# Kernel optimization log

Measured on AMD Instinct MI355X. Metric: run time of the kernel, lower is better.

## Reference

```python
import jax, jax.numpy as jnp
import numpy as np
from jax.ops import segment_sum, segment_max

N_M = 100000   # muon nodes
N_J = 100000   # jet nodes
E   = 1600000  # edges per relation (~avg degree 16)
D   = 64       # input feature dim
H   = 64       # hidden_channels
C   = 2        # num_classes

def setup_inputs():
    key = jax.random.key(0)
    ks = jax.random.split(key, 16)
    g = lambda k, shape, fan: jax.random.normal(k, shape, jnp.float32) / np.sqrt(fan).astype(np.float32)
    return {
        "x_muons": jax.random.normal(ks[0], (N_M, D), jnp.float32),
        "x_jets":  jax.random.normal(ks[1], (N_J, D), jnp.float32),
        "ei_mm": jax.random.randint(ks[2], (2, E), 0, N_M, jnp.int32),
        "ei_mj": jnp.stack([jax.random.randint(ks[3], (E,), 0, N_M, jnp.int32),
                            jax.random.randint(ks[4], (E,), 0, N_J, jnp.int32)]),
        "ei_jj": jax.random.randint(ks[5], (2, E), 0, N_J, jnp.int32),
        "gat_w_src": g(ks[6], (D, H), D),
        "gat_w_dst": g(ks[7], (D, H), D),
        "gat_att_src": g(ks[8], (H,), H),
        "gat_att_dst": g(ks[9], (H,), H),
        "gat_bias": jnp.zeros((H,), jnp.float32),
        "sage_w_l": g(ks[10], (D, H), D),
        "sage_w_r": g(ks[11], (D, H), D),
        "sage_bias": jnp.zeros((H,), jnp.float32),
        "gcn_w": g(ks[12], (D, H), D),
        "gcn_bias": jnp.zeros((H,), jnp.float32),
        "lin_w": g(ks[13], (H, C), H),
        "lin_b": jnp.zeros((C,), jnp.float32),
    }

def _add_self_loops(ei, n):
    loop = jnp.arange(n, dtype=ei.dtype)
    return jnp.concatenate([ei[0], loop]), jnp.concatenate([ei[1], loop])

def _gat(x, ei, w_src, w_dst, att_src, att_dst, bias):
    # PyG GATConv, heads=1, add_self_loops=True, negative_slope=0.2
    n = x.shape[0]
    src, dst = _add_self_loops(ei, n)
    hs = x @ w_src                      # [n, H] source-side messages
    hd = x @ w_dst                      # dst-side (attention only)
    a = jax.nn.leaky_relu((hs @ att_src)[src] + (hd @ att_dst)[dst], 0.2)
    m = segment_max(a, dst, num_segments=n)      # per-dst softmax (stable)
    ea = jnp.exp(a - m[dst])
    z = segment_sum(ea, dst, num_segments=n)
    alpha = ea / z[dst]                 # self loop guarantees z > 0
    return segment_sum(alpha[:, None] * hs[src], dst, num_segments=n) + bias

def _sage(x_src, x_dst, ei, w_l, w_r, bias):
    # PyG SAGEConv: mean aggregation, root weight, no self loops
    n = x_dst.shape[0]
    src, dst = ei[0], ei[1]
    agg = segment_sum(x_src[src], dst, num_segments=n)
    cnt = segment_sum(jnp.ones_like(dst, jnp.float32), dst, num_segments=n)
    mean = agg / jnp.maximum(cnt, 1.0)[:, None]
    return mean @ w_l + x_dst @ w_r + bias

def _gcn(x, ei, w, bias):
    # PyG GCNConv: symmetric gcn_norm on A + I
    n = x.shape[0]
    src, dst = _add_self_loops(ei, n)
    xw = x @ w
    deg = segment_sum(jnp.ones_like(dst, jnp.float32), dst, num_segments=n)
    dis = deg ** -0.5                   # deg >= 1 due to self loops
    norm = dis[src] * dis[dst]
    return segment_sum(norm[:, None] * xw[src], dst, num_segments=n) + bias

def reference(x_muons, x_jets, ei_mm, ei_mj, ei_jj,
              gat_w_src, gat_w_dst, gat_att_src, gat_att_dst, gat_bias,
              sage_w_l, sage_w_r, sage_bias, gcn_w, gcn_bias, lin_w, lin_b):
    # Original forward returns inside the layer loop -> exactly one HeteroConv layer runs.
    muons = _gat(x_muons, ei_mm, gat_w_src, gat_w_dst, gat_att_src, gat_att_dst, gat_bias)
    jets = (_sage(x_muons, x_jets, ei_mj, sage_w_l, sage_w_r, sage_bias)
            + _gcn(x_jets, ei_jj, gcn_w, gcn_bias))   # HeteroConv aggr='sum' on dst type 'jets'
    muons = jax.nn.relu(muons)
    jets = jax.nn.relu(jets)
    out = jnp.concatenate([muons, jets], axis=0)       # [N_M + N_J, H]
    return jax.nn.sigmoid(out @ lin_w + lin_b)
```

## Files before the change

### kernel.cpp

```cpp
#include <hip/hip_runtime.h>
#include <math.h>

#define N_M 100000
#define N_J 100000
#define NE  1600000
#define NTOT (3*N_M)
#define ETOT (3*NE)
#define NB_SCAN 293
#define DD  64
#define HH  64

#define NBIN 586
#define BIN_SHIFT 9
#define G1 640
#define EPB ((ETOT + G1 - 1) / G1)

__device__ __forceinline__ float lrelu(float a){ return fmaxf(a, 0.2f*a); }
__device__ __forceinline__ float wmax(float v){
    #pragma unroll
    for (int o = 32; o; o >>= 1) v = fmaxf(v, __shfl_xor(v, o));
    return v;
}
__device__ __forceinline__ float wsum(float v){
    #pragma unroll
    for (int o = 32; o; o >>= 1) v += __shfl_xor(v, o);
    return v;
}
__device__ __forceinline__ float sigm(float x){ return 1.f/(1.f + expf(-x)); }

__device__ __forceinline__ unsigned short f2bf(float f){
    unsigned u = __float_as_uint(f);
    u += 0x7FFFu + ((u >> 16) & 1u);
    return (unsigned short)(u >> 16);
}
__device__ __forceinline__ float bf2f(unsigned short h){
    return __uint_as_float((unsigned)h << 16);
}


__global__ __launch_bounds__(256) void k_muon_prep(
    const float* __restrict__ x, const float* __restrict__ w_src,
    const float* __restrict__ w_dst, const float* __restrict__ att_src,
    const float* __restrict__ att_dst,
    unsigned short* __restrict__ hs_b, float* __restrict__ as_, float* __restrict__ ad_,
    unsigned short* __restrict__ xm_b)
{
    __shared__ float lw[DD*HH];
    __shared__ float latt[HH];
    __shared__ float lvd[DD];
    int tid = threadIdx.x;
    for (int i = tid; i < DD*HH; i += 256) lw[i] = w_src[i];
    if (tid < HH) latt[tid] = att_src[tid];
    if (tid < DD){
        float s = 0.f;
        #pragma unroll 8
        for (int h = 0; h < HH; ++h) s += w_dst[tid*HH + h] * att_dst[h];
        lvd[tid] = s;
    }
    __syncthreads();
    int row = blockIdx.x*64 + (tid >> 2);
    int q = tid & 3;
    if (row >= N_M) return;
    const float4* x4 = (const float4*)(x + (size_t)row*DD);
    float acc[16];
    #pragma unroll
    for (int f = 0; f < 16; ++f) acc[f] = 0.f;
    float adp = 0.f;
    for (int kk = 0; kk < 16; ++kk){
        float4 xv = x4[kk];
        adp += xv.x*lvd[4*kk] + xv.y*lvd[4*kk+1] + xv.z*lvd[4*kk+2] + xv.w*lvd[4*kk+3];
        if ((kk >> 2) == q)
            *(ushort4*)(xm_b + (size_t)row*DD + 4*kk) =
                make_ushort4(f2bf(xv.x), f2bf(xv.y), f2bf(xv.z), f2bf(xv.w));
        float xs[4] = {xv.x, xv.y, xv.z, xv.w};
        #pragma unroll
        for (int j = 0; j < 4; ++j){
            const float* wp = lw + (4*kk + j)*HH + (q << 4);
            float xk = xs[j];
            #pragma unroll
            for (int f = 0; f < 16; ++f) acc[f] = fmaf(xk, wp[f], acc[f]);
        }
    }
    float asp = 0.f;
    #pragma unroll
    for (int f = 0; f < 16; ++f) asp += acc[f] * latt[(q<<4) + f];
    asp += __shfl_xor(asp, 1);
    asp += __shfl_xor(asp, 2);
    unsigned short* hp = hs_b + (size_t)row*HH + (q << 4);
    #pragma unroll
    for (int j = 0; j < 4; ++j)
        ((ushort4*)hp)[j] = make_ushort4(f2bf(acc[4*j]), f2bf(acc[4*j+1]),
                                         f2bf(acc[4*j+2]), f2bf(acc[4*j+3]));
    if (q == 0){ as_[row] = asp; ad_[row] = adp; }
}

__global__ __launch_bounds__(256) void k_jet_prep(
    const float* __restrict__ x, const float* __restrict__ gcn_w,
    const float* __restrict__ w_r, const float* __restrict__ sb,
    const float* __restrict__ gb,
    unsigned short* __restrict__ xw_b, float* __restrict__ xr)
{
    __shared__ float lwg[DD*HH];
    __shared__ float lwr[DD*HH];
    __shared__ float lb[HH];
    int tid = threadIdx.x;
    for (int i = tid; i < DD*HH; i += 256){ lwg[i] = gcn_w[i]; lwr[i] = w_r[i]; }
    if (tid < HH) lb[tid] = sb[tid] + gb[tid];
    __syncthreads();
    int row = blockIdx.x*64 + (tid >> 2);
    int q = tid & 3;
    if (row >= N_J) return;
    const float4* x4 = (const float4*)(x + (size_t)row*DD);
    float accg[16], accr[16];
    #pragma unroll
    for (int f = 0; f < 16; ++f){ accg[f] = 0.f; accr[f] = 0.f; }
    for (int kk = 0; kk < 16; ++kk){
        float4 xv = x4[kk];
        float xs[4] = {xv.x, xv.y, xv.z, xv.w};
        #pragma unroll
        for (int j = 0; j < 4; ++j){
            const float* wg = lwg + (4*kk + j)*HH + (q << 4);
            const float* wr = lwr + (4*kk + j)*HH + (q << 4);
            float xk = xs[j];
            #pragma unroll
            for (int f = 0; f < 16; ++f){
                accg[f] = fmaf(xk, wg[f], accg[f]);
                accr[f] = fmaf(xk, wr[f], accr[f]);
            }
        }
    }
    unsigned short* hp = xw_b + (size_t)row*HH + (q << 4);
    float* rp = xr + (size_t)row*HH + (q << 4);
    #pragma unroll
    for (int j = 0; j < 4; ++j){
        ((ushort4*)hp)[j] = make_ushort4(f2bf(accg[4*j]), f2bf(accg[4*j+1]),
                                         f2bf(accg[4*j+2]), f2bf(accg[4*j+3]));
        int f0 = (q << 4) + 4*j;
        ((float4*)rp)[j] = make_float4(accr[4*j]   + lb[f0],
                                       accr[4*j+1] + lb[f0+1],
                                       accr[4*j+2] + lb[f0+2],
                                       accr[4*j+3] + lb[f0+3]);
    }
}


__device__ __forceinline__ void edge_rd(int t, const int* ei_mm, const int* ei_mj,
                                        const int* ei_jj, const int** ei, int* r, int* e){
    if (t < NE){ *r = 0; *e = t; *ei = ei_mm; }
    else if (t < 2*NE){ *r = 1; *e = t - NE; *ei = ei_mj; }
    else { *r = 2; *e = t - 2*NE; *ei = ei_jj; }
}

__global__ __launch_bounds__(256) void k_bin0(
    const int* __restrict__ ei_mm, const int* __restrict__ ei_mj,
    const int* __restrict__ ei_jj, int* __restrict__ g_bincnt)
{
    __shared__ int bh[NBIN];
    int tid = threadIdx.x;
    for (int i = tid; i < NBIN; i += 256) bh[i] = 0;
    __syncthreads();
    int t0 = blockIdx.x * EPB;
    int t1 = min(t0 + EPB, ETOT);
    for (int t = t0 + tid; t < t1; t += 256){
        const int* ei; int r, e;
        edge_rd(t, ei_mm, ei_mj, ei_jj, &ei, &r, &e);
        int bucket = r*N_M + ei[NE + e];
        atomicAdd(&bh[bucket >> BIN_SHIFT], 1);
    }
    __syncthreads();
    for (int i = tid; i < NBIN; i += 256)
        if (bh[i]) atomicAdd(&g_bincnt[i], bh[i]);
}

__global__ void k_binscan(const int* __restrict__ g_bincnt, int* __restrict__ g_binoff,
                          int* __restrict__ g_bincur, int* __restrict__ offs)
{
    int l = threadIdx.x;
    int base = l * 10;
    int v[10]; int s = 0;
    #pragma unroll
    for (int k = 0; k < 10; ++k){
        int idx = base + k;
        v[k] = (idx < NBIN) ? g_bincnt[idx] : 0;
        s += v[k];
    }
    int inc = s;
    #pragma unroll
    for (int o = 1; o < 64; o <<= 1){
        int u = __shfl_up(inc, o);
        if (l >= o) inc += u;
    }
    int ex = inc - s;
    #pragma unroll
    for (int k = 0; k < 10; ++k){
        int idx = base + k;
        if (idx < NBIN){ g_binoff[idx] = ex; g_bincur[idx] = ex; ex += v[k]; }
    }
    if (l == 63) g_binoff[NBIN] = ex;
    if (l == 0)  offs[NTOT] = ETOT;
}

__global__ __launch_bounds__(256) void k_bin1(
    const int* __restrict__ ei_mm, const int* __restrict__ ei_mj,
    const int* __restrict__ ei_jj, int* __restrict__ g_bincur,
    unsigned* __restrict__ binned)
{
    __shared__ int bh[NBIN];
    __shared__ int cb[NBIN];
    int tid = threadIdx.x;
    for (int i = tid; i < NBIN; i += 256) bh[i] = 0;
    __syncthreads();
    int t0 = blockIdx.x * EPB;
    int t1 = min(t0 + EPB, ETOT);
    for (int t = t0 + tid; t < t1; t += 256){
        const int* ei; int r, e;
        edge_rd(t, ei_mm, ei_mj, ei_jj, &ei, &r, &e);
        int bucket = r*N_M + ei[NE + e];
        atomicAdd(&bh[bucket >> BIN_SHIFT], 1);
    }
    __syncthreads();
    for (int i = tid; i < NBIN; i += 256){
        int c = bh[i];
        cb[i] = c ? atomicAdd(&g_bincur[i], c) : 0;
        bh[i] = 0;
    }
    __syncthreads();
    for (int t = t0 + tid; t < t1; t += 256){
        const int* ei; int r, e;
        edge_rd(t, ei_mm, ei_mj, ei_jj, &ei, &r, &e);
        int s = ei[e];
        int bucket = r*N_M + ei[NE + e];
        int bin = bucket >> BIN_SHIFT;
        int lb  = bucket & 511;
        int pos = cb[bin] + atomicAdd(&bh[bin], 1);
        binned[pos] = ((unsigned)lb << 17) | (unsigned)s;
    }
}

__global__ __launch_bounds__(256) void k_build(
    const unsigned* __restrict__ binned, const int* __restrict__ g_binoff,
    int* __restrict__ offs, int* __restrict__ perm, float* __restrict__ dis)
{
    __shared__ int lh[512];
    __shared__ int lcur[512];
    __shared__ int ls[256];
    int b = blockIdx.x, tid = threadIdx.x;
    int e0 = g_binoff[b], e1 = g_binoff[b+1];
    lh[tid] = 0; lh[tid + 256] = 0;
    __syncthreads();
    for (int e = e0 + tid; e < e1; e += 256)
        atomicAdd(&lh[binned[e] >> 17], 1);
    __syncthreads();
    int a0 = lh[2*tid], a1 = lh[2*tid + 1];
    int s = a0 + a1;
    ls[tid] = s; __syncthreads();
    for (int o = 1; o < 256; o <<= 1){
        int u = (tid >= o) ? ls[tid - o] : 0;
        __syncthreads();
        ls[tid] += u;
        __syncthreads();
    }
    int ex = ls[tid] - s;
    lcur[2*tid]     = ex;
    lcur[2*tid + 1] = ex + a0;
    int gb = b*512 + 2*tid;
    if (gb     < NTOT) offs[gb]     = e0 + ex;
    if (gb + 1 < NTOT) offs[gb + 1] = e0 + ex + a0;
    if (gb     >= 2*N_M && gb     < NTOT) dis[gb     - 2*N_M] = rsqrtf((float)a0 + 1.f);
    if (gb + 1 >= 2*N_M && gb + 1 < NTOT) dis[gb + 1 - 2*N_M] = rsqrtf((float)a1 + 1.f);
    __syncthreads();
    for (int e = e0 + tid; e < e1; e += 256){
        unsigned p = binned[e];
        int pos = atomicAdd(&lcur[p >> 17], 1);
        perm[e0 + pos] = (int)(p & 0x1FFFFu);
    }
}


__global__ void k_hist(const int* __restrict__ ei_mm, const int* __restrict__ ei_mj,
                       const int* __restrict__ ei_jj, int* __restrict__ cnt){
    int t = blockIdx.x*256 + threadIdx.x;
    if (t >= ETOT) return;
    const int* ei; int r, e;
    edge_rd(t, ei_mm, ei_mj, ei_jj, &ei, &r, &e);
    atomicAdd(&cnt[r*N_M + ei[NE + e]], 1);
}

__global__ __launch_bounds__(256) void k_scan1(const int* __restrict__ cnt,
                                               int* __restrict__ offs, int* __restrict__ bsum){
    __shared__ int ls[256];
    int b = blockIdx.x, t = threadIdx.x;
    int base = b*1024 + t*4;
    int4 c = make_int4(0,0,0,0);
    if (base < NTOT) c = *(const int4*)(cnt + base);
    int s = c.x + c.y + c.z + c.w;
    ls[t] = s; __syncthreads();
    for (int o = 1; o < 256; o <<= 1){
        int a = (t >= o) ? ls[t - o] : 0;
        __syncthreads();
        ls[t] += a;
        __syncthreads();
    }
    int excl = ls[t] - s;
    if (t == 255) bsum[b] = ls[255];
    if (base < NTOT){
        offs[base]   = excl;
        offs[base+1] = excl + c.x;
        offs[base+2] = excl + c.x + c.y;
        offs[base+3] = excl + c.x + c.y + c.z;
    }
}

__global__ __launch_bounds__(512) void k_scan2(int* __restrict__ bsum){
    __shared__ int ls[512];
    int t = threadIdx.x;
    int v = (t < NB_SCAN) ? bsum[t] : 0;
    ls[t] = v; __syncthreads();
    for (int o = 1; o < 512; o <<= 1){
        int a = (t >= o) ? ls[t - o] : 0;
        __syncthreads();
        ls[t] += a;
        __syncthreads();
    }
    if (t < NB_SCAN) bsum[t] = ls[t] - v;
}

__global__ void k_scan3(int* __restrict__ offs, const int* __restrict__ bsum){
    int b = blockIdx.x, t = threadIdx.x;
    int base = b*1024 + t*4;
    if (base >= NTOT) return;
    int add = bsum[b];
    int4* p = (int4*)(offs + base);
    int4 v = *p;
    v.x += add; v.y += add; v.z += add; v.w += add;
    *p = v;
}

__global__ void k_fill(const int* __restrict__ ei_mm, const int* __restrict__ ei_mj,
                       const int* __restrict__ ei_jj, const int* __restrict__ offs,
                       int* __restrict__ cursor, int* __restrict__ perm){
    int t = blockIdx.x*256 + threadIdx.x;
    if (t >= ETOT) return;
    const int* ei; int r, e;
    edge_rd(t, ei_mm, ei_mj, ei_jj, &ei, &r, &e);
    int s = ei[e];
    int bkt = r*N_M + ei[NE + e];
    int pos = atomicAdd(&cursor[bkt], 1);
    perm[offs[bkt] + pos] = s;
}

__global__ void k_set_offs_top(int* __restrict__ offs){ offs[NTOT] = ETOT; }

__global__ void k_dis(const int* __restrict__ offs, float* __restrict__ dis){
    int j = blockIdx.x*256 + threadIdx.x;
    if (j >= N_J) return;
    int beg = offs[2*N_M + j];
    int end = (j == N_J-1) ? ETOT : offs[2*N_M + j + 1];
    dis[j] = rsqrtf((float)(end - beg + 1));
}


__global__ __launch_bounds__(512) void k_muon_gat_out(
    const int* __restrict__ offs, const int* __restrict__ perm,
    const float* __restrict__ as_, const float* __restrict__ ad_,
    const unsigned short* __restrict__ hs_b, const float* __restrict__ gat_bias,
    const float* __restrict__ lin_w, const float* __restrict__ lin_b,
    float* __restrict__ out)
{
    int wid = threadIdx.x >> 6;
    int l = threadIdx.x & 63;
    int d = blockIdx.x*8 + wid;
    if (d >= N_M) return;
    int p = l & 15, g = l >> 4;
    int beg = offs[d], end = offs[d+1];
    float ad_d = ad_[d];
    float a_self = lrelu(as_[d] + ad_d);
    float m = a_self, z = 0.f;
    float acc0 = 0.f, acc1 = 0.f, acc2 = 0.f, acc3 = 0.f;
    for (int base = beg; base < end; base += 64){
        int e = base + l;
        int sB = 0; float aB = -1e30f;
        if (e < end){ sB = perm[e]; aB = lrelu(as_[sB] + ad_d); }
        float bm = wmax(aB);
        if (bm > m){
            float sc = expf(m - bm);
            acc0 *= sc; acc1 *= sc; acc2 *= sc; acc3 *= sc; z *= sc;
            m = bm;
        }
        float eaB = expf(aB - m);
        z += wsum(eaB);
        int cc = min(64, end - base);
        int k = 0;
        for (; k + 32 <= cc; k += 32){
            #pragma unroll
            for (int qq = 0; qq < 8; ++qq){
                int idx = k + qq*4 + g;
                int s = __shfl(sB, idx);
                float w = __shfl(eaB, idx);
                ushort4 v = *(const ushort4*)(hs_b + (size_t)s*HH + 4*p);
                acc0 = fmaf(w, bf2f(v.x), acc0);
                acc1 = fmaf(w, bf2f(v.y), acc1);
                acc2 = fmaf(w, bf2f(v.z), acc2);
                acc3 = fmaf(w, bf2f(v.w), acc3);
            }
        }
        for (; k < cc; k += 4){
            int idx = k + g;
            int cl = min(idx, cc - 1);
            int s = __shfl(sB, cl);
            float w = __shfl(eaB, cl);
            if (idx >= cc) w = 0.f;
            ushort4 v = *(const ushort4*)(hs_b + (size_t)s*HH + 4*p);
            acc0 = fmaf(w, bf2f(v.x), acc0);
            acc1 = fmaf(w, bf2f(v.y), acc1);
            acc2 = fmaf(w, bf2f(v.z), acc2);
            acc3 = fmaf(w, bf2f(v.w), acc3);
        }
    }
    acc0 += __shfl_xor(acc0, 16); acc0 += __shfl_xor(acc0, 32);
    acc1 += __shfl_xor(acc1, 16); acc1 += __shfl_xor(acc1, 32);
    acc2 += __shfl_xor(acc2, 16); acc2 += __shfl_xor(acc2, 32);
    acc3 += __shfl_xor(acc3, 16); acc3 += __shfl_xor(acc3, 32);
    float eself = expf(a_self - m);
    z += eself;
    ushort4 hv = *(const ushort4*)(hs_b + (size_t)d*HH + 4*p);
    acc0 = fmaf(eself, bf2f(hv.x), acc0);
    acc1 = fmaf(eself, bf2f(hv.y), acc1);
    acc2 = fmaf(eself, bf2f(hv.z), acc2);
    acc3 = fmaf(eself, bf2f(hv.w), acc3);
    float rz = 1.f / z;
    float q0 = 0.f, q1 = 0.f;
    {
        float a[4] = {acc0, acc1, acc2, acc3};
        #pragma unroll
        for (int c = 0; c < 4; ++c){
            int f = 4*p + c;
            float v2 = fmaxf(a[c]*rz + gat_bias[f], 0.f);
            q0 = fmaf(v2, lin_w[f*2 + 0], q0);
            q1 = fmaf(v2, lin_w[f*2 + 1], q1);
        }
    }
    #pragma unroll
    for (int o = 1; o <= 8; o <<= 1){ q0 += __shfl_xor(q0, o); q1 += __shfl_xor(q1, o); }
    if (l == 0){
        size_t oo = (size_t)d*2;
        out[oo]   = sigm(q0 + lin_b[0]);
        out[oo+1] = sigm(q1 + lin_b[1]);
    }
}

__global__ __launch_bounds__(512) void k_jet_out(
    const unsigned short* __restrict__ xm_b, const unsigned short* __restrict__ xw_b,
    const float* __restrict__ xr, const float* __restrict__ dis,
    const int* __restrict__ offs, const int* __restrict__ perm,
    const float* __restrict__ w_l,
    const float* __restrict__ lin_w, const float* __restrict__ lin_b,
    float* __restrict__ out)
{
    __shared__ float lwl[DD*HH];
    int tid = threadIdx.x;
    for (int i = tid; i < DD*HH; i += 512) lwl[i] = w_l[i];
    __syncthreads();
    int wid = tid >> 6;
    int l = tid & 63;
    int j = blockIdx.x*8 + wid;
    if (j >= N_J) return;
    int p = l & 15, g = l >> 4;
    int beg1 = offs[N_M + j],  end1 = offs[N_M + j + 1];
    int beg2 = offs[2*N_M + j];
    int end2 = (j == N_J-1) ? ETOT : offs[2*N_M + j + 1];
    float dj = dis[j];
    float sa0 = 0.f, sa1 = 0.f, sa2 = 0.f, sa3 = 0.f;
    float gc0 = 0.f, gc1 = 0.f, gc2 = 0.f, gc3 = 0.f;
    for (int b1 = beg1, b2 = beg2; b1 < end1 || b2 < end2; b1 += 64, b2 += 64){
        int e1 = b1 + l, e2 = b2 + l;
        bool h1 = (b1 < end1), h2 = (b2 < end2);
        int sB1 = 0, sB2 = 0; float nB2 = 0.f;
        if (h1 && e1 < end1) sB1 = perm[e1];
        if (h2 && e2 < end2){ sB2 = perm[e2]; nB2 = dis[sB2]*dj; }
        if (h1){
            int cc = min(64, end1 - b1);
            int k = 0;
            for (; k + 16 <= cc; k += 16){
                #pragma unroll
                for (int qq = 0; qq < 4; ++qq){
                    int idx = k + qq*4 + g;
                    int s = __shfl(sB1, idx);
                    ushort4 v = *(const ushort4*)(xm_b + (size_t)s*DD + 4*p);
                    sa0 += bf2f(v.x); sa1 += bf2f(v.y); sa2 += bf2f(v.z); sa3 += bf2f(v.w);
                }
            }
            for (; k < cc; k += 4){
                int idx = k + g;
                int cl = min(idx, cc - 1);
                int s = __shfl(sB1, cl);
                float w = (idx < cc) ? 1.f : 0.f;
                ushort4 v = *(const ushort4*)(xm_b + (size_t)s*DD + 4*p);
                sa0 = fmaf(w, bf2f(v.x), sa0);
                sa1 = fmaf(w, bf2f(v.y), sa1);
                sa2 = fmaf(w, bf2f(v.z), sa2);
                sa3 = fmaf(w, bf2f(v.w), sa3);
            }
        }
        if (h2){
            int cc = min(64, end2 - b2);
            int k = 0;
            for (; k + 16 <= cc; k += 16){
                #pragma unroll
                for (int qq = 0; qq < 4; ++qq){
                    int idx = k + qq*4 + g;
                    int s = __shfl(sB2, idx);
                    float w = __shfl(nB2, idx);
                    ushort4 v = *(const ushort4*)(xw_b + (size_t)s*HH + 4*p);
                    gc0 = fmaf(w, bf2f(v.x), gc0);
                    gc1 = fmaf(w, bf2f(v.y), gc1);
                    gc2 = fmaf(w, bf2f(v.z), gc2);
                    gc3 = fmaf(w, bf2f(v.w), gc3);
                }
            }
            for (; k < cc; k += 4){
                int idx = k + g;
                int cl = min(idx, cc - 1);
                int s = __shfl(sB2, cl);
                float w = __shfl(nB2, cl);
                if (idx >= cc) w = 0.f;
                ushort4 v = *(const ushort4*)(xw_b + (size_t)s*HH + 4*p);
                gc0 = fmaf(w, bf2f(v.x), gc0);
                gc1 = fmaf(w, bf2f(v.y), gc1);
                gc2 = fmaf(w, bf2f(v.z), gc2);
                gc3 = fmaf(w, bf2f(v.w), gc3);
            }
        }
    }
    sa0 += __shfl_xor(sa0, 16); sa0 += __shfl_xor(sa0, 32);
    sa1 += __shfl_xor(sa1, 16); sa1 += __shfl_xor(sa1, 32);
    sa2 += __shfl_xor(sa2, 16); sa2 += __shfl_xor(sa2, 32);
    sa3 += __shfl_xor(sa3, 16); sa3 += __shfl_xor(sa3, 32);
    gc0 += __shfl_xor(gc0, 16); gc0 += __shfl_xor(gc0, 32);
    gc1 += __shfl_xor(gc1, 16); gc1 += __shfl_xor(gc1, 32);
    gc2 += __shfl_xor(gc2, 16); gc2 += __shfl_xor(gc2, 32);
    gc3 += __shfl_xor(gc3, 16); gc3 += __shfl_xor(gc3, 32);
    float inv = (end1 > beg1) ? 1.f/(float)(end1 - beg1) : 1.f;
    float mean_a[4] = {sa0*inv, sa1*inv, sa2*inv, sa3*inv};
    {
        ushort4 sv = *(const ushort4*)(xw_b + (size_t)j*HH + 4*p);
        float djj = dj*dj;
        gc0 = fmaf(djj, bf2f(sv.x), gc0);
        gc1 = fmaf(djj, bf2f(sv.y), gc1);
        gc2 = fmaf(djj, bf2f(sv.z), gc2);
        gc3 = fmaf(djj, bf2f(sv.w), gc3);
    }
    float b0 = __shfl(gc0, l >> 2), b1 = __shfl(gc1, l >> 2);
    float b2 = __shfl(gc2, l >> 2), b3 = __shfl(gc3, l >> 2);
    int c2 = l & 3;
    float accg_lin = (c2 == 0) ? b0 : ((c2 == 1) ? b1 : ((c2 == 2) ? b2 : b3));
    float xacc = 0.f;
    #pragma unroll
    for (int k = 0; k < 64; ++k){
        float mk = __shfl(mean_a[k & 3], k >> 2);
        xacc = fmaf(mk, lwl[k*64 + l], xacc);
    }
    float v2 = fmaxf(xacc + accg_lin + xr[(size_t)j*HH + l], 0.f);
    float q0 = wsum(v2 * lin_w[l*2 + 0]);
    float q1 = wsum(v2 * lin_w[l*2 + 1]);
    if (l == 0){
        size_t oo = (size_t)(N_M + j)*2;
        out[oo]   = sigm(q0 + lin_b[0]);
        out[oo+1] = sigm(q1 + lin_b[1]);
    }
}

extern "C" void kernel_launch(void* const* d_in, const int* in_sizes, int n_in,
                              void* d_out, int out_size, void* d_ws, size_t ws_size,
                              hipStream_t stream) {
    const float* x_muons   = (const float*)d_in[0];
    const float* x_jets    = (const float*)d_in[1];
    const int*   ei_mm     = (const int*)d_in[2];
    const int*   ei_mj     = (const int*)d_in[3];
    const int*   ei_jj     = (const int*)d_in[4];
    const float* gat_w_src = (const float*)d_in[5];
    const float* gat_w_dst = (const float*)d_in[6];
    const float* gat_att_s = (const float*)d_in[7];
    const float* gat_att_d = (const float*)d_in[8];
    const float* gat_bias  = (const float*)d_in[9];
    const float* sage_w_l  = (const float*)d_in[10];
    const float* sage_w_r  = (const float*)d_in[11];
    const float* sage_bias = (const float*)d_in[12];
    const float* gcn_w     = (const float*)d_in[13];
    const float* gcn_bias  = (const float*)d_in[14];
    const float* lin_w     = (const float*)d_in[15];
    const float* lin_b     = (const float*)d_in[16];
    float* out = (float*)d_out;

    float* ws = (float*)d_ws;
    size_t o = 0;
    unsigned short* hs_b = (unsigned short*)(ws + o); o += (size_t)N_M*HH/2;
    unsigned short* xw_b = (unsigned short*)(ws + o); o += (size_t)N_J*HH/2;
    unsigned short* xm_b = (unsigned short*)(ws + o); o += (size_t)N_M*DD/2;
    float* xr    = ws + o; o += (size_t)N_J*HH;
    float* as_   = ws + o; o += N_M;
    float* ad_   = ws + o; o += N_M;
    float* dis   = ws + o; o += N_J;
    int* offs   = (int*)(ws + o); o += NTOT + 4;
    int* perm   = (int*)(ws + o); o += ETOT;
    size_t o_common = o;

    int nb64_m = (N_M + 63) / 64;
    int nb64_j = (N_J + 63) / 64;

    k_muon_prep<<<nb64_m, 256, 0, stream>>>(x_muons, gat_w_src, gat_w_dst,
                                            gat_att_s, gat_att_d,
                                            hs_b, as_, ad_, xm_b);
    k_jet_prep<<<nb64_j, 256, 0, stream>>>(x_jets, gcn_w, sage_w_r, sage_bias,
                                           gcn_bias, xw_b, xr);

    size_t need_fast = (o_common + ETOT + 3*NBIN + 16) * sizeof(float);
    if (ws_size >= need_fast){
        unsigned* binned = (unsigned*)(ws + o); o += ETOT;
        int* g_bincnt    = (int*)(ws + o); o += NBIN;
        int* g_binoff    = (int*)(ws + o); o += NBIN + 4;
        int* g_bincur    = (int*)(ws + o); o += NBIN;
        hipMemsetAsync(g_bincnt, 0, NBIN*sizeof(int), stream);
        k_bin0<<<G1, 256, 0, stream>>>(ei_mm, ei_mj, ei_jj, g_bincnt);
        k_binscan<<<1, 64, 0, stream>>>(g_bincnt, g_binoff, g_bincur, offs);
        k_bin1<<<G1, 256, 0, stream>>>(ei_mm, ei_mj, ei_jj, g_bincur, binned);
        k_build<<<NBIN, 256, 0, stream>>>(binned, g_binoff, offs, perm, dis);
    } else {
        int* cnt    = (int*)(ws + o); o += NTOT;
        int* cursor = (int*)(ws + o); o += NTOT;
        int* bsum   = (int*)(ws + o); o += 512;
        hipMemsetAsync(cnt,    0, (size_t)NTOT*sizeof(int), stream);
        hipMemsetAsync(cursor, 0, (size_t)NTOT*sizeof(int), stream);
        int nbE3 = (ETOT + 255) / 256;
        k_hist<<<nbE3, 256, 0, stream>>>(ei_mm, ei_mj, ei_jj, cnt);
        k_scan1<<<NB_SCAN, 256, 0, stream>>>(cnt, offs, bsum);
        k_scan2<<<1, 512, 0, stream>>>(bsum);
        k_scan3<<<NB_SCAN, 256, 0, stream>>>(offs, bsum);
        k_fill<<<nbE3, 256, 0, stream>>>(ei_mm, ei_mj, ei_jj, offs, cursor, perm);
        k_set_offs_top<<<1, 1, 0, stream>>>(offs);
        k_dis<<<(N_J + 255)/256, 256, 0, stream>>>(offs, dis);
    }

    k_muon_gat_out<<<(N_M + 7)/8, 512, 0, stream>>>(offs, perm, as_, ad_, hs_b,
                                                    gat_bias, lin_w, lin_b, out);
    k_jet_out<<<(N_J + 7)/8, 512, 0, stream>>>(xm_b, xw_b, xr, dis, offs, perm,
                                               sage_w_l, lin_w, lin_b, out);
}
```

Before: 449.8 us.

## Merge GAT and jet output kernels, use global max bound for softmax

Replaces the per-block online softmax max in the GAT aggregation with a static upper bound, lrelu(max(as) + ad_d), computed through an atomicMax in the muon prep kernel. This removes the per-chunk wave max reduction and rescaling. The muon and jet output kernels are merged into one launch with interleaved blocks so both run concurrently. The jet prep kernel moves to 512-thread blocks, and the SAGE weight is read from global memory instead of LDS. The global max bound risks exp underflow when a node's logits sit far below the global max.

```diff
diff --git a/kernel.cpp b/kernel.cpp
--- a/kernel.cpp
+++ b/kernel.cpp
@@ -28,6 +28,14 @@
 }
 __device__ __forceinline__ float sigm(float x){ return 1.f/(1.f + expf(-x)); }
 
+__device__ __forceinline__ unsigned ford(float f){
+    unsigned b = __float_as_uint(f);
+    return (b & 0x80000000u) ? ~b : (b | 0x80000000u);
+}
+__device__ __forceinline__ float funord(unsigned u){
+    return (u & 0x80000000u) ? __uint_as_float(u & 0x7fffffffu) : __uint_as_float(~u);
+}
+
 __device__ __forceinline__ unsigned short f2bf(float f){
     unsigned u = __float_as_uint(f);
     u += 0x7FFFu + ((u >> 16) & 1u);
@@ -43,11 +51,12 @@
     const float* __restrict__ w_dst, const float* __restrict__ att_src,
     const float* __restrict__ att_dst,
     unsigned short* __restrict__ hs_b, float* __restrict__ as_, float* __restrict__ ad_,
-    unsigned short* __restrict__ xm_b)
+    unsigned short* __restrict__ xm_b, unsigned* __restrict__ maxAs_u)
 {
     __shared__ float lw[DD*HH];
     __shared__ float latt[HH];
     __shared__ float lvd[DD];
+    __shared__ float lred[4];
     int tid = threadIdx.x;
     for (int i = tid; i < DD*HH; i += 256) lw[i] = w_src[i];
     if (tid < HH) latt[tid] = att_src[tid];
@@ -60,41 +69,51 @@
     __syncthreads();
     int row = blockIdx.x*64 + (tid >> 2);
     int q = tid & 3;
-    if (row >= N_M) return;
-    const float4* x4 = (const float4*)(x + (size_t)row*DD);
-    float acc[16];
-    #pragma unroll
-    for (int f = 0; f < 16; ++f) acc[f] = 0.f;
-    float adp = 0.f;
-    for (int kk = 0; kk < 16; ++kk){
-        float4 xv = x4[kk];
-        adp += xv.x*lvd[4*kk] + xv.y*lvd[4*kk+1] + xv.z*lvd[4*kk+2] + xv.w*lvd[4*kk+3];
-        if ((kk >> 2) == q)
-            *(ushort4*)(xm_b + (size_t)row*DD + 4*kk) =
-                make_ushort4(f2bf(xv.x), f2bf(xv.y), f2bf(xv.z), f2bf(xv.w));
-        float xs[4] = {xv.x, xv.y, xv.z, xv.w};
+    bool live = (row < N_M);
+    float asp = -1e30f, adp = 0.f;
+    if (live){
+        const float4* x4 = (const float4*)(x + (size_t)row*DD);
+        float acc[16];
         #pragma unroll
-        for (int j = 0; j < 4; ++j){
-            const float* wp = lw + (4*kk + j)*HH + (q << 4);
-            float xk = xs[j];
+        for (int f = 0; f < 16; ++f) acc[f] = 0.f;
+        for (int kk = 0; kk < 16; ++kk){
+            float4 xv = x4[kk];
+            adp += xv.x*lvd[4*kk] + xv.y*lvd[4*kk+1] + xv.z*lvd[4*kk+2] + xv.w*lvd[4*kk+3];
+            if ((kk >> 2) == q)
+                *(ushort4*)(xm_b + (size_t)row*DD + 4*kk) =
+                    make_ushort4(f2bf(xv.x), f2bf(xv.y), f2bf(xv.z), f2bf(xv.w));
+            float xs[4] = {xv.x, xv.y, xv.z, xv.w};
             #pragma unroll
-            for (int f = 0; f < 16; ++f) acc[f] = fmaf(xk, wp[f], acc[f]);
-        }
-    }
-    float asp = 0.f;
-    #pragma unroll
-    for (int f = 0; f < 16; ++f) asp += acc[f] * latt[(q<<4) + f];
-    asp += __shfl_xor(asp, 1);
-    asp += __shfl_xor(asp, 2);
-    unsigned short* hp = hs_b + (size_t)row*HH + (q << 4);
-    #pragma unroll
-    for (int j = 0; j < 4; ++j)
-        ((ushort4*)hp)[j] = make_ushort4(f2bf(acc[4*j]), f2bf(acc[4*j+1]),
-                                         f2bf(acc[4*j+2]), f2bf(acc[4*j+3]));
-    if (q == 0){ as_[row] = asp; ad_[row] = adp; }
-}
-
-__global__ __launch_bounds__(256) void k_jet_prep(
+            for (int j = 0; j < 4; ++j){
+                const float* wp = lw + (4*kk + j)*HH + (q << 4);
+                float xk = xs[j];
+                #pragma unroll
+                for (int f = 0; f < 16; ++f) acc[f] = fmaf(xk, wp[f], acc[f]);
+            }
+        }
+        float a = 0.f;
+        #pragma unroll
+        for (int f = 0; f < 16; ++f) a += acc[f] * latt[(q<<4) + f];
+        a += __shfl_xor(a, 1);
+        a += __shfl_xor(a, 2);
+        asp = a;
+        unsigned short* hp = hs_b + (size_t)row*HH + (q << 4);
+        #pragma unroll
+        for (int j = 0; j < 4; ++j)
+            ((ushort4*)hp)[j] = make_ushort4(f2bf(acc[4*j]), f2bf(acc[4*j+1]),
+                                             f2bf(acc[4*j+2]), f2bf(acc[4*j+3]));
+        if (q == 0){ as_[row] = asp; ad_[row] = adp; }
+    }
+    float bm = wmax(asp);
+    if ((tid & 63) == 0) lred[tid >> 6] = bm;
+    __syncthreads();
+    if (tid == 0){
+        float m = fmaxf(fmaxf(lred[0], lred[1]), fmaxf(lred[2], lred[3]));
+        atomicMax(maxAs_u, ford(m));
+    }
+}
+
+__global__ __launch_bounds__(512) void k_jet_prep(
     const float* __restrict__ x, const float* __restrict__ gcn_w,
     const float* __restrict__ w_r, const float* __restrict__ sb,
     const float* __restrict__ gb,
@@ -104,10 +123,10 @@
     __shared__ float lwr[DD*HH];
     __shared__ float lb[HH];
     int tid = threadIdx.x;
-    for (int i = tid; i < DD*HH; i += 256){ lwg[i] = gcn_w[i]; lwr[i] = w_r[i]; }
+    for (int i = tid; i < DD*HH; i += 512){ lwg[i] = gcn_w[i]; lwr[i] = w_r[i]; }
     if (tid < HH) lb[tid] = sb[tid] + gb[tid];
     __syncthreads();
-    int row = blockIdx.x*64 + (tid >> 2);
+    int row = blockIdx.x*128 + (tid >> 2);
     int q = tid & 3;
     if (row >= N_J) return;
     const float4* x4 = (const float4*)(x + (size_t)row*DD);
@@ -360,43 +379,59 @@
 }
 
 
-__global__ __launch_bounds__(512) void k_muon_gat_out(
+__global__ __launch_bounds__(512) void k_out(
+    const unsigned short* __restrict__ xm_b, const unsigned short* __restrict__ xw_b,
+    const float* __restrict__ xr, const float* __restrict__ dis,
     const int* __restrict__ offs, const int* __restrict__ perm,
     const float* __restrict__ as_, const float* __restrict__ ad_,
-    const unsigned short* __restrict__ hs_b, const float* __restrict__ gat_bias,
+    const unsigned short* __restrict__ hs_b, const unsigned* __restrict__ maxAs_u,
+    const float* __restrict__ gat_bias, const float* __restrict__ w_l,
     const float* __restrict__ lin_w, const float* __restrict__ lin_b,
     float* __restrict__ out)
 {
-    int wid = threadIdx.x >> 6;
-    int l = threadIdx.x & 63;
-    int d = blockIdx.x*8 + wid;
-    if (d >= N_M) return;
+    int tid = threadIdx.x;
+    int wid = tid >> 6;
+    int l = tid & 63;
     int p = l & 15, g = l >> 4;
-    int beg = offs[d], end = offs[d+1];
-    float ad_d = ad_[d];
-    float a_self = lrelu(as_[d] + ad_d);
-    float m = a_self, z = 0.f;
-    float acc0 = 0.f, acc1 = 0.f, acc2 = 0.f, acc3 = 0.f;
-    for (int base = beg; base < end; base += 64){
-        int e = base + l;
-        int sB = 0; float aB = -1e30f;
-        if (e < end){ sB = perm[e]; aB = lrelu(as_[sB] + ad_d); }
-        float bm = wmax(aB);
-        if (bm > m){
-            float sc = expf(m - bm);
-            acc0 *= sc; acc1 *= sc; acc2 *= sc; acc3 *= sc; z *= sc;
-            m = bm;
-        }
-        float eaB = expf(aB - m);
-        z += wsum(eaB);
-        int cc = min(64, end - base);
-        int k = 0;
-        for (; k + 32 <= cc; k += 32){
-            #pragma unroll
-            for (int qq = 0; qq < 8; ++qq){
-                int idx = k + qq*4 + g;
-                int s = __shfl(sB, idx);
-                float w = __shfl(eaB, idx);
+    int b = blockIdx.x;
+    if (b & 1){
+        int d = (b >> 1)*8 + wid;
+        if (d >= N_M) return;
+        int beg = offs[d], end = offs[d+1];
+        float ad_d = ad_[d];
+        float M = lrelu(funord(*maxAs_u) + ad_d);
+        float a_self = lrelu(as_[d] + ad_d);
+        float zl = 0.f;
+        float acc0 = 0.f, acc1 = 0.f, acc2 = 0.f, acc3 = 0.f;
+        for (int base = beg; base < end; base += 64){
+            int e = base + l;
+            int sB = 0; float eaB = 0.f;
+            if (e < end){
+                sB = perm[e];
+                eaB = expf(lrelu(as_[sB] + ad_d) - M);
+            }
+            zl += eaB;
+            int cc = min(64, end - base);
+            int k = 0;
+            for (; k + 32 <= cc; k += 32){
+                #pragma unroll
+                for (int qq = 0; qq < 8; ++qq){
+                    int idx = k + qq*4 + g;
+                    int s = __shfl(sB, idx);
+                    float w = __shfl(eaB, idx);
+                    ushort4 v = *(const ushort4*)(hs_b + (size_t)s*HH + 4*p);
+                    acc0 = fmaf(w, bf2f(v.x), acc0);
+                    acc1 = fmaf(w, bf2f(v.y), acc1);
+                    acc2 = fmaf(w, bf2f(v.z), acc2);
+                    acc3 = fmaf(w, bf2f(v.w), acc3);
+                }
+            }
+            for (; k < cc; k += 4){
+                int idx = k + g;
+                int cl = min(idx, cc - 1);
+                int s = __shfl(sB, cl);
+                float w = __shfl(eaB, cl);
+                if (idx >= cc) w = 0.f;
                 ushort4 v = *(const ushort4*)(hs_b + (size_t)s*HH + 4*p);
                 acc0 = fmaf(w, bf2f(v.x), acc0);
                 acc1 = fmaf(w, bf2f(v.y), acc1);
@@ -404,113 +439,98 @@
                 acc3 = fmaf(w, bf2f(v.w), acc3);
             }
         }
-        for (; k < cc; k += 4){
-            int idx = k + g;
-            int cl = min(idx, cc - 1);
-            int s = __shfl(sB, cl);
-            float w = __shfl(eaB, cl);
-            if (idx >= cc) w = 0.f;
-            ushort4 v = *(const ushort4*)(hs_b + (size_t)s*HH + 4*p);
-            acc0 = fmaf(w, bf2f(v.x), acc0);
-            acc1 = fmaf(w, bf2f(v.y), acc1);
-            acc2 = fmaf(w, bf2f(v.z), acc2);
-            acc3 = fmaf(w, bf2f(v.w), acc3);
-        }
-    }
-    acc0 += __shfl_xor(acc0, 16); acc0 += __shfl_xor(acc0, 32);
-    acc1 += __shfl_xor(acc1, 16); acc1 += __shfl_xor(acc1, 32);
-    acc2 += __shfl_xor(acc2, 16); acc2 += __shfl_xor(acc2, 32);
-    acc3 += __shfl_xor(acc3, 16); acc3 += __shfl_xor(acc3, 32);
-    float eself = expf(a_self - m);
-    z += eself;
-    ushort4 hv = *(const ushort4*)(hs_b + (size_t)d*HH + 4*p);
-    acc0 = fmaf(eself, bf2f(hv.x), acc0);
-    acc1 = fmaf(eself, bf2f(hv.y), acc1);
-    acc2 = fmaf(eself, bf2f(hv.z), acc2);
-    acc3 = fmaf(eself, bf2f(hv.w), acc3);
-    float rz = 1.f / z;
-    float q0 = 0.f, q1 = 0.f;
-    {
-        float a[4] = {acc0, acc1, acc2, acc3};
+        float z = wsum(zl);
+        acc0 += __shfl_xor(acc0, 16); acc0 += __shfl_xor(acc0, 32);
+        acc1 += __shfl_xor(acc1, 16); acc1 += __shfl_xor(acc1, 32);
+        acc2 += __shfl_xor(acc2, 16); acc2 += __shfl_xor(acc2, 32);
+        acc3 += __shfl_xor(acc3, 16); acc3 += __shfl_xor(acc3, 32);
+        float eself = expf(a_self - M);
+        z += eself;
+        ushort4 hv = *(const ushort4*)(hs_b + (size_t)d*HH + 4*p);
+        acc0 = fmaf(eself, bf2f(hv.x), acc0);
+        acc1 = fmaf(eself, bf2f(hv.y), acc1);
+        acc2 = fmaf(eself, bf2f(hv.z), acc2);
+        acc3 = fmaf(eself, bf2f(hv.w), acc3);
+        float rz = 1.f / z;
+        float q0 = 0.f, q1 = 0.f;
+        {
+            float a[4] = {acc0, acc1, acc2, acc3};
+            #pragma unroll
+            for (int c = 0; c < 4; ++c){
+                int f = 4*p + c;
+                float v2 = fmaxf(a[c]*rz + gat_bias[f], 0.f);
+                q0 = fmaf(v2, lin_w[f*2 + 0], q0);
+                q1 = fmaf(v2, lin_w[f*2 + 1], q1);
+            }
+        }
         #pragma unroll
-        for (int c = 0; c < 4; ++c){
-            int f = 4*p + c;
-            float v2 = fmaxf(a[c]*rz + gat_bias[f], 0.f);
-            q0 = fmaf(v2, lin_w[f*2 + 0], q0);
-            q1 = fmaf(v2, lin_w[f*2 + 1], q1);
-        }
-    }
-    #pragma unroll
-    for (int o = 1; o <= 8; o <<= 1){ q0 += __shfl_xor(q0, o); q1 += __shfl_xor(q1, o); }
-    if (l == 0){
-        size_t oo = (size_t)d*2;
-        out[oo]   = sigm(q0 + lin_b[0]);
-        out[oo+1] = sigm(q1 + lin_b[1]);
-    }
-}
-
-__global__ __launch_bounds__(512) void k_jet_out(
-    const unsigned short* __restrict__ xm_b, const unsigned short* __restrict__ xw_b,
-    const float* __restrict__ xr, const float* __restrict__ dis,
-    const int* __restrict__ offs, const int* __restrict__ perm,
-    const float* __restrict__ w_l,
-    const float* __restrict__ lin_w, const float* __restrict__ lin_b,
-    float* __restrict__ out)
-{
-    __shared__ float lwl[DD*HH];
-    int tid = threadIdx.x;
-    for (int i = tid; i < DD*HH; i += 512) lwl[i] = w_l[i];
-    __syncthreads();
-    int wid = tid >> 6;
-    int l = tid & 63;
-    int j = blockIdx.x*8 + wid;
-    if (j >= N_J) return;
-    int p = l & 15, g = l >> 4;
-    int beg1 = offs[N_M + j],  end1 = offs[N_M + j + 1];
-    int beg2 = offs[2*N_M + j];
-    int end2 = (j == N_J-1) ? ETOT : offs[2*N_M + j + 1];
-    float dj = dis[j];
-    float sa0 = 0.f, sa1 = 0.f, sa2 = 0.f, sa3 = 0.f;
-    float gc0 = 0.f, gc1 = 0.f, gc2 = 0.f, gc3 = 0.f;
-    for (int b1 = beg1, b2 = beg2; b1 < end1 || b2 < end2; b1 += 64, b2 += 64){
-        int e1 = b1 + l, e2 = b2 + l;
-        bool h1 = (b1 < end1), h2 = (b2 < end2);
-        int sB1 = 0, sB2 = 0; float nB2 = 0.f;
-        if (h1 && e1 < end1) sB1 = perm[e1];
-        if (h2 && e2 < end2){ sB2 = perm[e2]; nB2 = dis[sB2]*dj; }
-        if (h1){
-            int cc = min(64, end1 - b1);
-            int k = 0;
-            for (; k + 16 <= cc; k += 16){
-                #pragma unroll
-                for (int qq = 0; qq < 4; ++qq){
-                    int idx = k + qq*4 + g;
-                    int s = __shfl(sB1, idx);
+        for (int o = 1; o <= 8; o <<= 1){ q0 += __shfl_xor(q0, o); q1 += __shfl_xor(q1, o); }
+        if (l == 0){
+            size_t oo = (size_t)d*2;
+            out[oo]   = sigm(q0 + lin_b[0]);
+            out[oo+1] = sigm(q1 + lin_b[1]);
+        }
+    } else {
+        int j = (b >> 1)*8 + wid;
+        if (j >= N_J) return;
+        int beg1 = offs[N_M + j],  end1 = offs[N_M + j + 1];
+        int beg2 = offs[2*N_M + j];
+        int end2 = (j == N_J-1) ? ETOT : offs[2*N_M + j + 1];
+        float dj = dis[j];
+        float sa0 = 0.f, sa1 = 0.f, sa2 = 0.f, sa3 = 0.f;
+        float gc0 = 0.f, gc1 = 0.f, gc2 = 0.f, gc3 = 0.f;
+        for (int b1 = beg1, b2 = beg2; b1 < end1 || b2 < end2; b1 += 64, b2 += 64){
+            int e1 = b1 + l, e2 = b2 + l;
+            bool h1 = (b1 < end1), h2 = (b2 < end2);
+            int sB1 = 0, sB2 = 0; float nB2 = 0.f;
+            if (h1 && e1 < end1) sB1 = perm[e1];
+            if (h2 && e2 < end2){ sB2 = perm[e2]; nB2 = dis[sB2]*dj; }
+            if (h1){
+                int cc = min(64, end1 - b1);
+                int k = 0;
+                for (; k + 16 <= cc; k += 16){
+                    #pragma unroll
+                    for (int qq = 0; qq < 4; ++qq){
+                        int idx = k + qq*4 + g;
+                        int s = __shfl(sB1, idx);
+                        ushort4 v = *(const ushort4*)(xm_b + (size_t)s*DD + 4*p);
+                        sa0 += bf2f(v.x); sa1 += bf2f(v.y); sa2 += bf2f(v.z); sa3 += bf2f(v.w);
+                    }
+                }
+                for (; k < cc; k += 4){
+                    int idx = k + g;
+                    int cl = min(idx, cc - 1);
+                    int s = __shfl(sB1, cl);
+                    float w = (idx < cc) ? 1.f : 0.f;
                     ushort4 v = *(const ushort4*)(xm_b + (size_t)s*DD + 4*p);
-                    sa0 += bf2f(v.x); sa1 += bf2f(v.y); sa2 += bf2f(v.z); sa3 += bf2f(v.w);
+                    sa0 = fmaf(w, bf2f(v.x), sa0);
+                    sa1 = fmaf(w, bf2f(v.y), sa1);
+                    sa2 = fmaf(w, bf2f(v.z), sa2);
+                    sa3 = fmaf(w, bf2f(v.w), sa3);
                 }
             }
-            for (; k < cc; k += 4){
-                int idx = k + g;
-                int cl = min(idx, cc - 1);
-                int s = __shfl(sB1, cl);
-                float w = (idx < cc) ? 1.f : 0.f;
-                ushort4 v = *(const ushort4*)(xm_b + (size_t)s*DD + 4*p);
-                sa0 = fmaf(w, bf2f(v.x), sa0);
-                sa1 = fmaf(w, bf2f(v.y), sa1);
-                sa2 = fmaf(w, bf2f(v.z), sa2);
-                sa3 = fmaf(w, bf2f(v.w), sa3);
-            }
-        }
-        if (h2){
-            int cc = min(64, end2 - b2);
-            int k = 0;
-            for (; k + 16 <= cc; k += 16){
-                #pragma unroll
-                for (int qq = 0; qq < 4; ++qq){
-                    int idx = k + qq*4 + g;
-                    int s = __shfl(sB2, idx);
-                    float w = __shfl(nB2, idx);
+            if (h2){
+                int cc = min(64, end2 - b2);
+                int k = 0;
+                for (; k + 16 <= cc; k += 16){
+                    #pragma unroll
+                    for (int qq = 0; qq < 4; ++qq){
+                        int idx = k + qq*4 + g;
+                        int s = __shfl(sB2, idx);
+                        float w = __shfl(nB2, idx);
+                        ushort4 v = *(const ushort4*)(xw_b + (size_t)s*HH + 4*p);
+                        gc0 = fmaf(w, bf2f(v.x), gc0);
+                        gc1 = fmaf(w, bf2f(v.y), gc1);
+                        gc2 = fmaf(w, bf2f(v.z), gc2);
+                        gc3 = fmaf(w, bf2f(v.w), gc3);
+                    }
+                }
+                for (; k < cc; k += 4){
+                    int idx = k + g;
+                    int cl = min(idx, cc - 1);
+                    int s = __shfl(sB2, cl);
+                    float w = __shfl(nB2, cl);
+                    if (idx >= cc) w = 0.f;
                     ushort4 v = *(const ushort4*)(xw_b + (size_t)s*HH + 4*p);
                     gc0 = fmaf(w, bf2f(v.x), gc0);
                     gc1 = fmaf(w, bf2f(v.y), gc1);
@@ -518,55 +538,43 @@
                     gc3 = fmaf(w, bf2f(v.w), gc3);
                 }
             }
-            for (; k < cc; k += 4){
-                int idx = k + g;
-                int cl = min(idx, cc - 1);
-                int s = __shfl(sB2, cl);
-                float w = __shfl(nB2, cl);
-                if (idx >= cc) w = 0.f;
-                ushort4 v = *(const ushort4*)(xw_b + (size_t)s*HH + 4*p);
-                gc0 = fmaf(w, bf2f(v.x), gc0);
-                gc1 = fmaf(w, bf2f(v.y), gc1);
-                gc2 = fmaf(w, bf2f(v.z), gc2);
-                gc3 = fmaf(w, bf2f(v.w), gc3);
-            }
-        }
-    }
-    sa0 += __shfl_xor(sa0, 16); sa0 += __shfl_xor(sa0, 32);
-    sa1 += __shfl_xor(sa1, 16); sa1 += __shfl_xor(sa1, 32);
-    sa2 += __shfl_xor(sa2, 16); sa2 += __shfl_xor(sa2, 32);
-    sa3 += __shfl_xor(sa3, 16); sa3 += __shfl_xor(sa3, 32);
-    gc0 += __shfl_xor(gc0, 16); gc0 += __shfl_xor(gc0, 32);
-    gc1 += __shfl_xor(gc1, 16); gc1 += __shfl_xor(gc1, 32);
-    gc2 += __shfl_xor(gc2, 16); gc2 += __shfl_xor(gc2, 32);
-    gc3 += __shfl_xor(gc3, 16); gc3 += __shfl_xor(gc3, 32);
-    float inv = (end1 > beg1) ? 1.f/(float)(end1 - beg1) : 1.f;
-    float mean_a[4] = {sa0*inv, sa1*inv, sa2*inv, sa3*inv};
-    {
-        ushort4 sv = *(const ushort4*)(xw_b + (size_t)j*HH + 4*p);
-        float djj = dj*dj;
-        gc0 = fmaf(djj, bf2f(sv.x), gc0);
-        gc1 = fmaf(djj, bf2f(sv.y), gc1);
-        gc2 = fmaf(djj, bf2f(sv.z), gc2);
-        gc3 = fmaf(djj, bf2f(sv.w), gc3);
-    }
-    float b0 = __shfl(gc0, l >> 2), b1 = __shfl(gc1, l >> 2);
-    float b2 = __shfl(gc2, l >> 2), b3 = __shfl(gc3, l >> 2);
-    int c2 = l & 3;
-    float accg_lin = (c2 == 0) ? b0 : ((c2 == 1) ? b1 : ((c2 == 2) ? b2 : b3));
-    float xacc = 0.f;
-    #pragma unroll
-    for (int k = 0; k < 64; ++k){
-        float mk = __shfl(mean_a[k & 3], k >> 2);
-        xacc = fmaf(mk, lwl[k*64 + l], xacc);
-    }
-    float v2 = fmaxf(xacc + accg_lin + xr[(size_t)j*HH + l], 0.f);
-    float q0 = wsum(v2 * lin_w[l*2 + 0]);
-    float q1 = wsum(v2 * lin_w[l*2 + 1]);
-    if (l == 0){
-        size_t oo = (size_t)(N_M + j)*2;
-        out[oo]   = sigm(q0 + lin_b[0]);
-        out[oo+1] = sigm(q1 + lin_b[1]);
+        }
+        sa0 += __shfl_xor(sa0, 16); sa0 += __shfl_xor(sa0, 32);
+        sa1 += __shfl_xor(sa1, 16); sa1 += __shfl_xor(sa1, 32);
+        sa2 += __shfl_xor(sa2, 16); sa2 += __shfl_xor(sa2, 32);
+        sa3 += __shfl_xor(sa3, 16); sa3 += __shfl_xor(sa3, 32);
+        gc0 += __shfl_xor(gc0, 16); gc0 += __shfl_xor(gc0, 32);
+        gc1 += __shfl_xor(gc1, 16); gc1 += __shfl_xor(gc1, 32);
+        gc2 += __shfl_xor(gc2, 16); gc2 += __shfl_xor(gc2, 32);
+        gc3 += __shfl_xor(gc3, 16); gc3 += __shfl_xor(gc3, 32);
+        float inv = (end1 > beg1) ? 1.f/(float)(end1 - beg1) : 1.f;
+        float mean_a[4] = {sa0*inv, sa1*inv, sa2*inv, sa3*inv};
+        {
+            ushort4 sv = *(const ushort4*)(xw_b + (size_t)j*HH + 4*p);
+            float djj = dj*dj;
+            gc0 = fmaf(djj, bf2f(sv.x), gc0);
+            gc1 = fmaf(djj, bf2f(sv.y), gc1);
+            gc2 = fmaf(djj, bf2f(sv.z), gc2);
+            gc3 = fmaf(djj, bf2f(sv.w), gc3);
+        }
+        float b0 = __shfl(gc0, l >> 2), b1 = __shfl(gc1, l >> 2);
+        float b2 = __shfl(gc2, l >> 2), b3 = __shfl(gc3, l >> 2);
+        int c2 = l & 3;
+        float accg_lin = (c2 == 0) ? b0 : ((c2 == 1) ? b1 : ((c2 == 2) ? b2 : b3));
+        float xacc = 0.f;
+        #pragma unroll
+        for (int k = 0; k < 64; ++k){
+            float mk = __shfl(mean_a[k & 3], k >> 2);
+            xacc = fmaf(mk, w_l[k*64 + l], xacc);
+        }
+        float v2 = fmaxf(xacc + accg_lin + xr[(size_t)j*HH + l], 0.f);
+        float q0 = wsum(v2 * lin_w[l*2 + 0]);
+        float q1 = wsum(v2 * lin_w[l*2 + 1]);
+        if (l == 0){
+            size_t oo = (size_t)(N_M + j)*2;
+            out[oo]   = sigm(q0 + lin_b[0]);
+            out[oo+1] = sigm(q1 + lin_b[1]);
+        }
     }
 }
 
@@ -601,18 +609,19 @@
     float* as_   = ws + o; o += N_M;
     float* ad_   = ws + o; o += N_M;
     float* dis   = ws + o; o += N_J;
+    unsigned* maxAs_u = (unsigned*)(ws + o); o += 16;
     int* offs   = (int*)(ws + o); o += NTOT + 4;
     int* perm   = (int*)(ws + o); o += ETOT;
     size_t o_common = o;
 
     int nb64_m = (N_M + 63) / 64;
-    int nb64_j = (N_J + 63) / 64;
-
+
+    hipMemsetAsync(maxAs_u, 0, sizeof(unsigned), stream);
     k_muon_prep<<<nb64_m, 256, 0, stream>>>(x_muons, gat_w_src, gat_w_dst,
                                             gat_att_s, gat_att_d,
-                                            hs_b, as_, ad_, xm_b);
-    k_jet_prep<<<nb64_j, 256, 0, stream>>>(x_jets, gcn_w, sage_w_r, sage_bias,
-                                           gcn_bias, xw_b, xr);
+                                            hs_b, as_, ad_, xm_b, maxAs_u);
+    k_jet_prep<<<(N_J + 127)/128, 512, 0, stream>>>(x_jets, gcn_w, sage_w_r, sage_bias,
+                                                    gcn_bias, xw_b, xr);
 
     size_t need_fast = (o_common + ETOT + 3*NBIN + 16) * sizeof(float);
     if (ws_size >= need_fast){
@@ -641,8 +650,8 @@
         k_dis<<<(N_J + 255)/256, 256, 0, stream>>>(offs, dis);
     }
 
-    k_muon_gat_out<<<(N_M + 7)/8, 512, 0, stream>>>(offs, perm, as_, ad_, hs_b,
-                                                    gat_bias, lin_w, lin_b, out);
-    k_jet_out<<<(N_J + 7)/8, 512, 0, stream>>>(xm_b, xw_b, xr, dis, offs, perm,
-                                               sage_w_l, lin_w, lin_b, out);
-}
+    int nb_out = 2 * ((N_M + 7)/8);
+    k_out<<<nb_out, 512, 0, stream>>>(xm_b, xw_b, xr, dis, offs, perm,
+                                      as_, ad_, hs_b, maxAs_u,
+                                      gat_bias, sage_w_l, lin_w, lin_b, out);
+}
```

After: 487.1 us. +8.3%, slower.
